# Performance work log

Hardware: AMD Instinct MI355X
Metric: run time of the kernel (lower is better)

The kernel has to match this reference:

```python
import jax, jax.numpy as jnp
import numpy as np

N_NODES = 50000
N_EDGES = 800000
IN_DIM = 128
HID = 32
HEADS = 4
EMB = 64
NEG_SLOPE = 0.2
LN_EPS = 1e-5


def setup_inputs() -> dict:
    key = jax.random.key(0)
    ks = jax.random.split(key, 16)
    s = 0.1
    inp = {
        'x': jax.random.normal(ks[0], (N_NODES, IN_DIM), dtype=jnp.float32),
        'edge_index': jax.random.randint(ks[1], (2, N_EDGES), 0, N_NODES, dtype=jnp.int64),
        # GATConv 1: in=128 -> heads=4, out_per_head=32, concat -> 128
        'W1': jax.random.normal(ks[2], (IN_DIM, HEADS * HID), dtype=jnp.float32) * s,
        'att_src1': jax.random.normal(ks[3], (HEADS, HID), dtype=jnp.float32) * s,
        'att_dst1': jax.random.normal(ks[4], (HEADS, HID), dtype=jnp.float32) * s,
        'b1': jnp.zeros((HEADS * HID,), dtype=jnp.float32),
        'gamma1': jnp.ones((HEADS * HID,), dtype=jnp.float32),
        'beta1': jnp.zeros((HEADS * HID,), dtype=jnp.float32),
        # GATConv 2: in=128 -> heads=1, out=64, concat=False
        'W2': jax.random.normal(ks[5], (HEADS * HID, EMB), dtype=jnp.float32) * s,
        'att_src2': jax.random.normal(ks[6], (1, EMB), dtype=jnp.float32) * s,
        'att_dst2': jax.random.normal(ks[7], (1, EMB), dtype=jnp.float32) * s,
        'b2': jnp.zeros((EMB,), dtype=jnp.float32),
        'gamma2': jnp.ones((EMB,), dtype=jnp.float32),
        'beta2': jnp.zeros((EMB,), dtype=jnp.float32),
    }
    return inp


def _gat_conv(x, src, dst, W, att_src, att_dst):
    # x: [N, F_in]; src/dst: [E'] (self loops included); W: [F_in, H*C]
    N = x.shape[0]
    H, C = att_src.shape
    h = (x @ W).reshape(N, H, C)                          # [N, H, C]
    a_s = jnp.sum(h * att_src, axis=-1)                   # [N, H]
    a_d = jnp.sum(h * att_dst, axis=-1)                   # [N, H]
    e = jax.nn.leaky_relu(a_s[src] + a_d[dst], NEG_SLOPE) # [E', H]
    # segment softmax over destination-node neighborhoods
    m = jax.ops.segment_max(e, dst, num_segments=N)       # [N, H]
    ex = jnp.exp(e - m[dst])
    den = jax.ops.segment_sum(ex, dst, num_segments=N)    # [N, H]
    alpha = ex / den[dst]                                  # [E', H]
    msg = h[src] * alpha[:, :, None]                       # [E', H, C]
    return jax.ops.segment_sum(msg, dst, num_segments=N)  # [N, H, C]


def _layer_norm(x, gamma, beta):
    mu = jnp.mean(x, axis=-1, keepdims=True)
    var = jnp.var(x, axis=-1, keepdims=True)
    return (x - mu) * jax.lax.rsqrt(var + LN_EPS) * gamma + beta


def reference(x, edge_index, W1, att_src1, att_dst1, b1, gamma1, beta1,
              W2, att_src2, att_dst2, b2, gamma2, beta2):
    N = x.shape[0]
    loops = jnp.arange(N, dtype=edge_index.dtype)
    src = jnp.concatenate([edge_index[0], loops])  # PyG add_self_loops=True
    dst = jnp.concatenate([edge_index[1], loops])

    # gat1: heads=4, concat=True
    h1 = _gat_conv(x, src, dst, W1, att_src1, att_dst1)   # [N, 4, 32]
    h1 = h1.reshape(N, -1) + b1                            # [N, 128]
    h1 = jax.nn.relu(_layer_norm(h1, gamma1, beta1))
    # dropout is identity in eval mode

    # gat2: heads=1, concat=False (mean over the single head)
    h2 = _gat_conv(h1, src, dst, W2, att_src2, att_dst2)  # [N, 1, 64]
    h2 = h2.mean(axis=1) + b2                              # [N, 64]
    return _layer_norm(h2, gamma2, beta2)
```

## Files before the change

### kernel.cpp

```cpp
#include <hip/hip_runtime.h>
#include <hip/hip_bf16.h>
#include <math.h>

#define N_NODES 50000
#define N_EDGES 800000
#define HEADS 4
#define HID 32
#define D1 128
#define D2 64
#define NEG_SLOPE 0.2f
#define LN_EPS 1e-5f

#define NB_SCAN ((N_NODES + 255) / 256)
#define CAP 64
#define GB1N 782
#define GB2N 782
#define DEGB 784
#define ILV (2 * GB1N)

typedef __attribute__((ext_vector_type(8))) short bf16x8;
typedef __attribute__((ext_vector_type(4))) float f32x4;

__device__ __forceinline__ float lrelu(float x) { return x > 0.f ? x : NEG_SLOPE * x; }
__device__ __forceinline__ float bf2f(__hip_bfloat16 v) { return __bfloat162float(v); }

__device__ __forceinline__ short f2bf_s(float x) {
    union { __hip_bfloat16 h; short s; } u;
    u.h = __float2bfloat16(x);
    return u.s;
}
__device__ __forceinline__ float bfs2f(short s) {
    union { unsigned u; float f; } v;
    v.u = ((unsigned)(unsigned short)s) << 16;
    return v.f;
}
__device__ __forceinline__ void split_bf(float x, short& hi, short& lo) {
    hi = f2bf_s(x);
    lo = f2bf_s(x - bfs2f(hi));
}

__global__ __launch_bounds__(256) void wprep_kernel(const float* __restrict__ W1,
                                                    const float* __restrict__ W2,
                                                    short* __restrict__ W1h, short* __restrict__ W1l,
                                                    short* __restrict__ W2h, short* __restrict__ W2l) {
    int idx = blockIdx.x * 256 + threadIdx.x;
    if (idx < 16384) {
        int s = idx & 7, l = (idx >> 3) & 63, fid = idx >> 9;
        int kt = fid & 3, nt = fid >> 2;
        int k = kt * 32 + (l >> 4) * 8 + s;
        int n = nt * 16 + (l & 15);
        short hi, lo;
        split_bf(W1[k * 128 + n], hi, lo);
        W1h[idx] = hi;
        W1l[idx] = lo;
    } else if (idx < 16384 + 8192) {
        int j = idx - 16384;
        int s = j & 7, l = (j >> 3) & 63, fid = j >> 9;
        int kt = fid & 3, nt = fid >> 2;
        int k = kt * 32 + (l >> 4) * 8 + s;
        int n = nt * 16 + (l & 15);
        short hi, lo;
        split_bf(W2[k * 64 + n], hi, lo);
        W2h[j] = hi;
        W2l[j] = lo;
    }
}

__global__ __launch_bounds__(256, 3) void gemm1_mfma_degree_kernel(
    const float* __restrict__ X, const short* __restrict__ Wh, const short* __restrict__ Wl,
    __hip_bfloat16* __restrict__ Y,
    const float* __restrict__ att_src, const float* __restrict__ att_dst,
    float* __restrict__ a_s, float* __restrict__ a_d,
    const int* __restrict__ dst, int* __restrict__ deg, int* __restrict__ rank) {
    int bid = blockIdx.x;
    bool isdeg;
    int id;
    if (bid < ILV) {
        isdeg = (bid & 1);
        id = bid >> 1;
    } else {
        isdeg = true;
        id = bid - ILV + GB1N;
    }
    if (isdeg) {
        int t0 = id * 256 + threadIdx.x;
        const int stride = DEGB * 256;
#pragma unroll
        for (int u = 0; u < 4; ++u) {
            int i = t0 + u * stride;
            if (i < N_EDGES) rank[i] = atomicAdd(&deg[dst[i]], 1);
        }
        return;
    }

    int tid = threadIdx.x;
    int w = tid >> 6;
    int l = tid & 63;
    int lr = l & 15;
    int lq = l >> 4;

    const bf16x8* Wh8 = (const bf16x8*)Wh;
    const bf16x8* Wl8 = (const bf16x8*)Wl;
    bf16x8 bh[2][4], bl[2][4];
#pragma unroll
    for (int nt = 0; nt < 2; ++nt)
#pragma unroll
        for (int kt = 0; kt < 4; ++kt) {
            int fid = (2 * w + nt) * 4 + kt;
            bh[nt][kt] = Wh8[fid * 64 + l];
            bl[nt][kt] = Wl8[fid * 64 + l];
        }

    int r0 = id * 64;
    float asv0 = att_src[w * 32 + lr], asv1 = att_src[w * 32 + 16 + lr];
    float adv0 = att_dst[w * 32 + lr], adv1 = att_dst[w * 32 + 16 + lr];

#pragma unroll
    for (int mt = 0; mt < 4; ++mt) {
        int rb = r0 + mt * 16;
        int row = rb + lr;
        if (row >= N_NODES) row = N_NODES - 1;
        const float* xr = X + (size_t)row * 128;
        f32x4 acc0 = {0.f, 0.f, 0.f, 0.f};
        f32x4 acc1 = {0.f, 0.f, 0.f, 0.f};
#pragma unroll
        for (int kt = 0; kt < 4; ++kt) {
            int cb = kt * 32 + lq * 8;
            float4 f0 = *(const float4*)(xr + cb);
            float4 f1 = *(const float4*)(xr + cb + 4);
            float xs[8] = {f0.x, f0.y, f0.z, f0.w, f1.x, f1.y, f1.z, f1.w};
            bf16x8 ah, al;
#pragma unroll
            for (int s = 0; s < 8; ++s) {
                short h_, l_;
                split_bf(xs[s], h_, l_);
                ah[s] = h_;
                al[s] = l_;
            }
            acc0 = __builtin_amdgcn_mfma_f32_16x16x32_bf16(ah, bh[0][kt], acc0, 0, 0, 0);
            acc1 = __builtin_amdgcn_mfma_f32_16x16x32_bf16(ah, bh[1][kt], acc1, 0, 0, 0);
            acc0 = __builtin_amdgcn_mfma_f32_16x16x32_bf16(al, bh[0][kt], acc0, 0, 0, 0);
            acc1 = __builtin_amdgcn_mfma_f32_16x16x32_bf16(al, bh[1][kt], acc1, 0, 0, 0);
            acc0 = __builtin_amdgcn_mfma_f32_16x16x32_bf16(ah, bl[0][kt], acc0, 0, 0, 0);
            acc1 = __builtin_amdgcn_mfma_f32_16x16x32_bf16(ah, bl[1][kt], acc1, 0, 0, 0);
        }
#pragma unroll
        for (int reg = 0; reg < 4; ++reg) {
            int r = rb + lq * 4 + reg;
            float v0 = acc0[reg], v1 = acc1[reg];
            float ps = v0 * asv0 + v1 * asv1;
            float pd = v0 * adv0 + v1 * adv1;
#pragma unroll
            for (int m = 1; m < 16; m <<= 1) {
                ps += __shfl_xor(ps, m, 64);
                pd += __shfl_xor(pd, m, 64);
            }
            if (r < N_NODES) {
                Y[(size_t)r * 128 + w * 32 + lr] = __float2bfloat16(v0);
                Y[(size_t)r * 128 + w * 32 + 16 + lr] = __float2bfloat16(v1);
                if (lr == 0) {
                    a_s[r * 4 + w] = ps;
                    a_d[r * 4 + w] = pd;
                }
            }
        }
    }
}

__global__ __launch_bounds__(256, 3) void gemm2_mfma_kernel(
    const float* __restrict__ X, const short* __restrict__ Wh, const short* __restrict__ Wl,
    __hip_bfloat16* __restrict__ Y,
    const float* __restrict__ att_src, const float* __restrict__ att_dst,
    float* __restrict__ a_s, float* __restrict__ a_d) {
    __shared__ float psh[4][64];
    __shared__ float pdh[4][64];
    int tid = threadIdx.x;
    int w = tid >> 6;
    int l = tid & 63;
    int lr = l & 15;
    int lq = l >> 4;

    const bf16x8* Wh8 = (const bf16x8*)Wh;
    const bf16x8* Wl8 = (const bf16x8*)Wl;
    bf16x8 bh[4], bl[4];
#pragma unroll
    for (int kt = 0; kt < 4; ++kt) {
        int fid = w * 4 + kt;
        bh[kt] = Wh8[fid * 64 + l];
        bl[kt] = Wl8[fid * 64 + l];
    }

    int r0 = blockIdx.x * 64;
    float asv = att_src[w * 16 + lr];
    float adv = att_dst[w * 16 + lr];

    f32x4 acc[4];
#pragma unroll
    for (int mt = 0; mt < 4; ++mt) acc[mt] = (f32x4){0.f, 0.f, 0.f, 0.f};

#pragma unroll
    for (int mt = 0; mt < 4; ++mt) {
        int row = r0 + mt * 16 + lr;
        if (row >= N_NODES) row = N_NODES - 1;
        const float* xr = X + (size_t)row * 128;
#pragma unroll
        for (int kt = 0; kt < 4; ++kt) {
            int cb = kt * 32 + lq * 8;
            float4 f0 = *(const float4*)(xr + cb);
            float4 f1 = *(const float4*)(xr + cb + 4);
            float xs[8] = {f0.x, f0.y, f0.z, f0.w, f1.x, f1.y, f1.z, f1.w};
            bf16x8 ah, al;
#pragma unroll
            for (int s = 0; s < 8; ++s) {
                short h_, l_;
                split_bf(xs[s], h_, l_);
                ah[s] = h_;
                al[s] = l_;
            }
            acc[mt] = __builtin_amdgcn_mfma_f32_16x16x32_bf16(ah, bh[kt], acc[mt], 0, 0, 0);
            acc[mt] = __builtin_amdgcn_mfma_f32_16x16x32_bf16(al, bh[kt], acc[mt], 0, 0, 0);
            acc[mt] = __builtin_amdgcn_mfma_f32_16x16x32_bf16(ah, bl[kt], acc[mt], 0, 0, 0);
        }
    }

#pragma unroll
    for (int mt = 0; mt < 4; ++mt) {
#pragma unroll
        for (int reg = 0; reg < 4; ++reg) {
            int r = r0 + mt * 16 + lq * 4 + reg;
            float v = acc[mt][reg];
            float ps = v * asv;
            float pd = v * adv;
#pragma unroll
            for (int m = 1; m < 16; m <<= 1) {
                ps += __shfl_xor(ps, m, 64);
                pd += __shfl_xor(pd, m, 64);
            }
            if (r < N_NODES) Y[(size_t)r * 64 + w * 16 + lr] = __float2bfloat16(v);
            if (lr == 0) {
                psh[w][mt * 16 + lq * 4 + reg] = ps;
                pdh[w][mt * 16 + lq * 4 + reg] = pd;
            }
        }
    }
    __syncthreads();
    if (tid < 64) {
        int r = r0 + tid;
        if (r < N_NODES) {
            a_s[r] = psh[0][tid] + psh[1][tid] + psh[2][tid] + psh[3][tid];
            a_d[r] = pdh[0][tid] + pdh[1][tid] + pdh[2][tid] + pdh[3][tid];
        }
    }
}

__global__ __launch_bounds__(256) void scan1_kernel(const int* __restrict__ deg,
                                                    int* __restrict__ rpl,
                                                    int* __restrict__ bsum) {
    int i = blockIdx.x * 256 + threadIdx.x;
    int v = (i < N_NODES) ? deg[i] : 0;
    int lane = threadIdx.x & 63;
    int w = threadIdx.x >> 6;
    int x = v;
#pragma unroll
    for (int off = 1; off < 64; off <<= 1) {
        int t = __shfl_up(x, off, 64);
        if (lane >= off) x += t;
    }
    __shared__ int wsum[4];
    if (lane == 63) wsum[w] = x;
    __syncthreads();
    int wo = 0;
    if (w > 0) wo += wsum[0];
    if (w > 1) wo += wsum[1];
    if (w > 2) wo += wsum[2];
    if (i <= N_NODES) rpl[i] = x - v + wo;
    if (threadIdx.x == 255) bsum[blockIdx.x] = x + wo;
}

__global__ __launch_bounds__(256) void scan2_kernel(const int* __restrict__ bsum,
                                                    int* __restrict__ boff) {
    int i = threadIdx.x;
    int v = (i < NB_SCAN) ? bsum[i] : 0;
    int lane = threadIdx.x & 63;
    int w = threadIdx.x >> 6;
    int x = v;
#pragma unroll
    for (int off = 1; off < 64; off <<= 1) {
        int t = __shfl_up(x, off, 64);
        if (lane >= off) x += t;
    }
    __shared__ int wsum[4];
    if (lane == 63) wsum[w] = x;
    __syncthreads();
    int wo = 0;
    if (w > 0) wo += wsum[0];
    if (w > 1) wo += wsum[1];
    if (w > 2) wo += wsum[2];
    if (i < NB_SCAN) boff[i] = x - v + wo;
}

__global__ __launch_bounds__(256) void scatter_kernel(const int* __restrict__ src,
                                                      const int* __restrict__ dst,
                                                      const int* __restrict__ rpl,
                                                      const int* __restrict__ boff,
                                                      const int* __restrict__ rank,
                                                      int* __restrict__ col) {
    int i = blockIdx.x * blockDim.x + threadIdx.x;
    if (i < N_EDGES) {
        int d = dst[i];
        int pos = rpl[d] + boff[d >> 8] + rank[i];
        col[pos] = src[i];
    }
}

__global__ __launch_bounds__(256) void agg1_kernel(const __hip_bfloat16* __restrict__ h,
                                                   const float* __restrict__ a_s,
                                                   const float* __restrict__ a_d,
                                                   const int* __restrict__ rpl,
                                                   const int* __restrict__ boff,
                                                   const int* __restrict__ col,
                                                   const float* __restrict__ b1,
                                                   const float* __restrict__ gamma,
                                                   const float* __restrict__ beta,
                                                   float* __restrict__ out) {
    __shared__ int colsh[4][CAP];
    __shared__ float wsh[4][CAP * 4];
    int wv = threadIdx.x >> 6;
    int lane = threadIdx.x & 63;
    int n = blockIdx.x * 4 + wv;
    int nn = (n < N_NODES) ? n : N_NODES - 1;
    int head = lane >> 4;
    int c = 2 * lane;

    const float4 ad4 = *(const float4*)&a_d[nn * 4];
    int beg = rpl[nn] + boff[nn >> 8];
    int end = rpl[nn + 1] + boff[(nn + 1) >> 8];
    int deg = end - beg;

    float den0 = 0.f, den1 = 0.f, den2 = 0.f, den3 = 0.f;
    for (int t = lane; t < deg; t += 64) {
        int s = col[beg + t];
        const float4 as4 = *(const float4*)&a_s[s * 4];
        float w0 = __expf(lrelu(as4.x + ad4.x));
        float w1 = __expf(lrelu(as4.y + ad4.y));
        float w2 = __expf(lrelu(as4.z + ad4.z));
        float w3 = __expf(lrelu(as4.w + ad4.w));
        if (t < CAP) {
            colsh[wv][t] = s;
            *(float4*)&wsh[wv][t * 4] = make_float4(w0, w1, w2, w3);
        }
        den0 += w0; den1 += w1; den2 += w2; den3 += w3;
    }
#pragma unroll
    for (int m = 1; m < 64; m <<= 1) {
        den0 += __shfl_xor(den0, m, 64);
        den1 += __shfl_xor(den1, m, 64);
        den2 += __shfl_xor(den2, m, 64);
        den3 += __shfl_xor(den3, m, 64);
    }
    float adh = (head == 0) ? ad4.x : (head == 1) ? ad4.y : (head == 2) ? ad4.z : ad4.w;
    float wself = __expf(lrelu(a_s[nn * 4 + head] + adh));
    float den = ((head == 0) ? den0 : (head == 1) ? den1 : (head == 2) ? den2 : den3) + wself;

    __syncthreads();

    float ax0 = 0.f, ay0 = 0.f, ax1 = 0.f, ay1 = 0.f;
    int m0 = (deg < CAP) ? deg : CAP;
    int j = 0;
    for (; j + 3 < m0; j += 4) {
        int s0 = colsh[wv][j + 0], s1 = colsh[wv][j + 1];
        int s2 = colsh[wv][j + 2], s3 = colsh[wv][j + 3];
        float w0 = wsh[wv][(j + 0) * 4 + head], w1 = wsh[wv][(j + 1) * 4 + head];
        float w2 = wsh[wv][(j + 2) * 4 + head], w3 = wsh[wv][(j + 3) * 4 + head];
        __hip_bfloat162 h0 = ((const __hip_bfloat162*)h)[(size_t)s0 * 64 + lane];
        __hip_bfloat162 h1 = ((const __hip_bfloat162*)h)[(size_t)s1 * 64 + lane];
        __hip_bfloat162 h2v = ((const __hip_bfloat162*)h)[(size_t)s2 * 64 + lane];
        __hip_bfloat162 h3 = ((const __hip_bfloat162*)h)[(size_t)s3 * 64 + lane];
        ax0 += w0 * bf2f(h0.x); ay0 += w0 * bf2f(h0.y);
        ax1 += w1 * bf2f(h1.x); ay1 += w1 * bf2f(h1.y);
        ax0 += w2 * bf2f(h2v.x); ay0 += w2 * bf2f(h2v.y);
        ax1 += w3 * bf2f(h3.x); ay1 += w3 * bf2f(h3.y);
    }
    for (; j < m0; ++j) {
        int s = colsh[wv][j];
        float w = wsh[wv][j * 4 + head];
        __hip_bfloat162 hv = ((const __hip_bfloat162*)h)[(size_t)s * 64 + lane];
        ax0 += w * bf2f(hv.x); ay0 += w * bf2f(hv.y);
    }
    for (; j < deg; ++j) {
        int s = col[beg + j];
        float w = __expf(lrelu(a_s[s * 4 + head] + adh));
        __hip_bfloat162 hv = ((const __hip_bfloat162*)h)[(size_t)s * 64 + lane];
        ax0 += w * bf2f(hv.x); ay0 += w * bf2f(hv.y);
    }
    {
        __hip_bfloat162 hv = ((const __hip_bfloat162*)h)[(size_t)nn * 64 + lane];
        ax0 += wself * bf2f(hv.x); ay0 += wself * bf2f(hv.y);
    }
    float inv = 1.f / den;
    float vx = (ax0 + ax1) * inv + b1[c];
    float vy = (ay0 + ay1) * inv + b1[c + 1];

    float s1 = vx + vy, s2 = vx * vx + vy * vy;
#pragma unroll
    for (int m = 1; m < 64; m <<= 1) {
        s1 += __shfl_xor(s1, m, 64);
        s2 += __shfl_xor(s2, m, 64);
    }
    float mean = s1 * (1.f / 128.f);
    float var = s2 * (1.f / 128.f) - mean * mean;
    float r = rsqrtf(var + LN_EPS);
    float ox = fmaxf(0.f, (vx - mean) * r * gamma[c] + beta[c]);
    float oy = fmaxf(0.f, (vy - mean) * r * gamma[c + 1] + beta[c + 1]);
    if (n < N_NODES) *(float2*)&out[(size_t)n * 128 + c] = make_float2(ox, oy);
}

__global__ __launch_bounds__(256) void agg2_kernel(const __hip_bfloat16* __restrict__ h,
                                                   const float* __restrict__ a_s,
                                                   const float* __restrict__ a_d,
                                                   const int* __restrict__ rpl,
                                                   const int* __restrict__ boff,
                                                   const int* __restrict__ col,
                                                   const float* __restrict__ b2,
                                                   const float* __restrict__ gamma,
                                                   const float* __restrict__ beta,
                                                   float* __restrict__ out) {
    __shared__ int colsh[4][CAP];
    __shared__ float wsh[4][CAP];
    int wv = threadIdx.x >> 6;
    int lane = threadIdx.x & 63;
    int n = blockIdx.x * 4 + wv;
    int nn = (n < N_NODES) ? n : N_NODES - 1;

    float adh = a_d[nn];
    int beg = rpl[nn] + boff[nn >> 8];
    int end = rpl[nn + 1] + boff[(nn + 1) >> 8];
    int deg = end - beg;

    float den = 0.f;
    for (int t = lane; t < deg; t += 64) {
        int s = col[beg + t];
        float w = __expf(lrelu(a_s[s] + adh));
        if (t < CAP) {
            colsh[wv][t] = s;
            wsh[wv][t] = w;
        }
        den += w;
    }
#pragma unroll
    for (int m = 1; m < 64; m <<= 1) den += __shfl_xor(den, m, 64);
    float wself = __expf(lrelu(a_s[nn] + adh));
    den += wself;

    __syncthreads();

    float a0 = 0.f, a1 = 0.f;
    int m0 = (deg < CAP) ? deg : CAP;
    int j = 0;
    for (; j + 3 < m0; j += 4) {
        int s0 = colsh[wv][j + 0], s1 = colsh[wv][j + 1];
        int s2 = colsh[wv][j + 2], s3 = colsh[wv][j + 3];
        float w0 = wsh[wv][j + 0], w1 = wsh[wv][j + 1];
        float w2 = wsh[wv][j + 2], w3 = wsh[wv][j + 3];
        a0 += w0 * bf2f(h[(size_t)s0 * 64 + lane]);
        a1 += w1 * bf2f(h[(size_t)s1 * 64 + lane]);
        a0 += w2 * bf2f(h[(size_t)s2 * 64 + lane]);
        a1 += w3 * bf2f(h[(size_t)s3 * 64 + lane]);
    }
    for (; j < m0; ++j) {
        a0 += wsh[wv][j] * bf2f(h[(size_t)colsh[wv][j] * 64 + lane]);
    }
    for (; j < deg; ++j) {
        int s = col[beg + j];
        float w = __expf(lrelu(a_s[s] + adh));
        a0 += w * bf2f(h[(size_t)s * 64 + lane]);
    }
    a0 += wself * bf2f(h[(size_t)nn * 64 + lane]);

    float v = (a0 + a1) / den + b2[lane];

    float s1 = v, s2 = v * v;
#pragma unroll
    for (int m = 1; m < 64; m <<= 1) {
        s1 += __shfl_xor(s1, m, 64);
        s2 += __shfl_xor(s2, m, 64);
    }
    float mean = s1 * (1.f / 64.f);
    float var = s2 * (1.f / 64.f) - mean * mean;
    float r = rsqrtf(var + LN_EPS);
    if (n < N_NODES) out[(size_t)n * 64 + lane] = (v - mean) * r * gamma[lane] + beta[lane];
}

extern "C" void kernel_launch(void* const* d_in, const int* in_sizes, int n_in,
                              void* d_out, int out_size, void* d_ws, size_t ws_size,
                              hipStream_t stream) {
    const float* x        = (const float*)d_in[0];
    const int*   ei       = (const int*)d_in[1];
    const float* W1       = (const float*)d_in[2];
    const float* att_src1 = (const float*)d_in[3];
    const float* att_dst1 = (const float*)d_in[4];
    const float* b1       = (const float*)d_in[5];
    const float* gamma1   = (const float*)d_in[6];
    const float* beta1    = (const float*)d_in[7];
    const float* W2       = (const float*)d_in[8];
    const float* att_src2 = (const float*)d_in[9];
    const float* att_dst2 = (const float*)d_in[10];
    const float* b2       = (const float*)d_in[11];
    const float* gamma2   = (const float*)d_in[12];
    const float* beta2    = (const float*)d_in[13];
    const int* src = ei;
    const int* dst = ei + N_EDGES;
    float* out = (float*)d_out;

    char* ws = (char*)d_ws;
    size_t off = 0;
    auto alloc = [&](size_t bytes) -> void* {
        void* p = ws + off;
        off += bytes;
        off = (off + 255) & ~(size_t)255;
        return p;
    };
    __hip_bfloat16* h1pre = (__hip_bfloat16*)alloc((size_t)N_NODES * 128 * 2);
    __hip_bfloat16* h2pre = (__hip_bfloat16*)alloc((size_t)N_NODES * 64 * 2);
    float* a_s1   = (float*)alloc((size_t)N_NODES * 4 * 4);
    float* a_d1   = (float*)alloc((size_t)N_NODES * 4 * 4);
    float* h1n    = (float*)alloc((size_t)N_NODES * 128 * 4);
    float* a_s2   = (float*)alloc((size_t)N_NODES * 4);
    float* a_d2   = (float*)alloc((size_t)N_NODES * 4);
    int* deg      = (int*)alloc((size_t)N_NODES * 4);
    int* rpl      = (int*)alloc((size_t)(N_NODES + 1) * 4);
    int* col      = (int*)alloc((size_t)N_EDGES * 4);
    int* rank     = (int*)alloc((size_t)N_EDGES * 4);
    int* bsum     = (int*)alloc((size_t)NB_SCAN * 4);
    int* boff     = (int*)alloc((size_t)NB_SCAN * 4);
    short* W1h    = (short*)alloc((size_t)16384 * 2);
    short* W1l    = (short*)alloc((size_t)16384 * 2);
    short* W2h    = (short*)alloc((size_t)8192 * 2);
    short* W2l    = (short*)alloc((size_t)8192 * 2);

    hipMemsetAsync(deg, 0, (size_t)N_NODES * 4, stream);

    const int EB = (N_EDGES + 255) / 256;
    const int NWB = (N_NODES + 3) / 4;

    wprep_kernel<<<96, 256, 0, stream>>>(W1, W2, W1h, W1l, W2h, W2l);

    gemm1_mfma_degree_kernel<<<GB1N + DEGB, 256, 0, stream>>>(
        x, W1h, W1l, h1pre, att_src1, att_dst1, a_s1, a_d1, dst, deg, rank);
    scan1_kernel<<<NB_SCAN, 256, 0, stream>>>(deg, rpl, bsum);
    scan2_kernel<<<1, 256, 0, stream>>>(bsum, boff);
    scatter_kernel<<<EB, 256, 0, stream>>>(src, dst, rpl, boff, rank, col);

    agg1_kernel<<<NWB, 256, 0, stream>>>(h1pre, a_s1, a_d1, rpl, boff, col, b1, gamma1, beta1, h1n);

    gemm2_mfma_kernel<<<GB2N, 256, 0, stream>>>(
        h1n, W2h, W2l, h2pre, att_src2, att_dst2, a_s2, a_d2);
    agg2_kernel<<<NWB, 256, 0, stream>>>(h2pre, a_s2, a_d2, rpl, boff, col, b2, gamma2, beta2, out);
}
```

Measured before the change: 249.6 us.

## Replace global-atomic degree count with per-chunk LDS histograms and sorted scatter

The CSR build drops the per-edge global atomicAdd on degree counts and the per-edge rank array. It now uses 256 edge chunks, each building a packed 16-bit-per-node histogram in shared memory, a column-wise exclusive scan across chunks, and a scatter that re-runs the LDS atomics to get local ranks. The goal is to remove global atomic contention and the rank write/read traffic. In exchange it adds a 25.6 MB histogram buffer that is written, scanned and read again, and the degree computation is no longer interleaved with gemm1.

```diff
diff --git a/kernel.cpp b/kernel.cpp
--- a/kernel.cpp
+++ b/kernel.cpp
@@ -15,8 +15,11 @@
 #define CAP 64
 #define GB1N 782
 #define GB2N 782
-#define DEGB 784
-#define ILV (2 * GB1N)
+
+#define NCHUNK 256
+#define CHE (N_EDGES / NCHUNK)
+#define HWORDS (N_NODES / 2)
+#define HVEC (HWORDS / 4)
 
 typedef __attribute__((ext_vector_type(8))) short bf16x8;
 typedef __attribute__((ext_vector_type(4))) float f32x4;
@@ -66,33 +69,61 @@
     }
 }
 
-__global__ __launch_bounds__(256, 3) void gemm1_mfma_degree_kernel(
+__global__ __launch_bounds__(512) void hist_kernel(const int* __restrict__ dst,
+                                                   unsigned* __restrict__ hist) {
+    __shared__ unsigned cnt[HWORDS];
+    int c = blockIdx.x;
+    for (int i = threadIdx.x; i < HVEC; i += 512) ((uint4*)cnt)[i] = make_uint4(0, 0, 0, 0);
+    __syncthreads();
+    int base = c * CHE;
+    for (int t = threadIdx.x; t < CHE; t += 512) {
+        int d = dst[base + t];
+        atomicAdd(&cnt[d >> 1], 1u << ((d & 1) * 16));
+    }
+    __syncthreads();
+    uint4* out = (uint4*)(hist + (size_t)c * HWORDS);
+    for (int i = threadIdx.x; i < HVEC; i += 512) out[i] = ((const uint4*)cnt)[i];
+}
+
+__global__ __launch_bounds__(256) void chunkscan_kernel(unsigned* __restrict__ hist,
+                                                        unsigned* __restrict__ degp) {
+    int w = blockIdx.x * 256 + threadIdx.x;
+    if (w >= HWORDS) return;
+    unsigned run = 0;
+#pragma unroll 8
+    for (int c = 0; c < NCHUNK; ++c) {
+        unsigned v = hist[(size_t)c * HWORDS + w];
+        hist[(size_t)c * HWORDS + w] = run;
+        run += v;
+    }
+    degp[w] = run;
+}
+
+__global__ __launch_bounds__(512) void scatter_sorted_kernel(const int* __restrict__ src,
+                                                             const int* __restrict__ dst,
+                                                             const unsigned* __restrict__ hist,
+                                                             const int* __restrict__ rpl,
+                                                             const int* __restrict__ boff,
+                                                             int* __restrict__ col) {
+    __shared__ unsigned cnt[HWORDS];
+    int c = blockIdx.x;
+    const uint4* row = (const uint4*)(hist + (size_t)c * HWORDS);
+    for (int i = threadIdx.x; i < HVEC; i += 512) ((uint4*)cnt)[i] = row[i];
+    __syncthreads();
+    int base = c * CHE;
+    for (int t = threadIdx.x; t < CHE; t += 512) {
+        int d = dst[base + t];
+        unsigned old = atomicAdd(&cnt[d >> 1], 1u << ((d & 1) * 16));
+        unsigned r = (old >> ((d & 1) * 16)) & 0xffffu;
+        col[rpl[d] + boff[d >> 8] + (int)r] = src[base + t];
+    }
+}
+
+__global__ __launch_bounds__(256, 3) void gemm1_mfma_kernel(
     const float* __restrict__ X, const short* __restrict__ Wh, const short* __restrict__ Wl,
     __hip_bfloat16* __restrict__ Y,
     const float* __restrict__ att_src, const float* __restrict__ att_dst,
-    float* __restrict__ a_s, float* __restrict__ a_d,
-    const int* __restrict__ dst, int* __restrict__ deg, int* __restrict__ rank) {
-    int bid = blockIdx.x;
-    bool isdeg;
-    int id;
-    if (bid < ILV) {
-        isdeg = (bid & 1);
-        id = bid >> 1;
-    } else {
-        isdeg = true;
-        id = bid - ILV + GB1N;
-    }
-    if (isdeg) {
-        int t0 = id * 256 + threadIdx.x;
-        const int stride = DEGB * 256;
-#pragma unroll
-        for (int u = 0; u < 4; ++u) {
-            int i = t0 + u * stride;
-            if (i < N_EDGES) rank[i] = atomicAdd(&deg[dst[i]], 1);
-        }
-        return;
-    }
-
+    float* __restrict__ a_s, float* __restrict__ a_d) {
     int tid = threadIdx.x;
     int w = tid >> 6;
     int l = tid & 63;
@@ -111,7 +142,7 @@
             bl[nt][kt] = Wl8[fid * 64 + l];
         }
 
-    int r0 = id * 64;
+    int r0 = blockIdx.x * 64;
     float asv0 = att_src[w * 32 + lr], asv1 = att_src[w * 32 + 16 + lr];
     float adv0 = att_dst[w * 32 + lr], adv1 = att_dst[w * 32 + 16 + lr];
 
@@ -253,11 +284,12 @@
     }
 }
 
-__global__ __launch_bounds__(256) void scan1_kernel(const int* __restrict__ deg,
+__global__ __launch_bounds__(256) void scan1_kernel(const unsigned* __restrict__ degp,
                                                     int* __restrict__ rpl,
                                                     int* __restrict__ bsum) {
     int i = blockIdx.x * 256 + threadIdx.x;
-    int v = (i < N_NODES) ? deg[i] : 0;
+    int v = 0;
+    if (i < N_NODES) v = (int)((degp[i >> 1] >> ((i & 1) * 16)) & 0xffffu);
     int lane = threadIdx.x & 63;
     int w = threadIdx.x >> 6;
     int x = v;
@@ -297,20 +329,6 @@
     if (w > 1) wo += wsum[1];
     if (w > 2) wo += wsum[2];
     if (i < NB_SCAN) boff[i] = x - v + wo;
-}
-
-__global__ __launch_bounds__(256) void scatter_kernel(const int* __restrict__ src,
-                                                      const int* __restrict__ dst,
-                                                      const int* __restrict__ rpl,
-                                                      const int* __restrict__ boff,
-                                                      const int* __restrict__ rank,
-                                                      int* __restrict__ col) {
-    int i = blockIdx.x * blockDim.x + threadIdx.x;
-    if (i < N_EDGES) {
-        int d = dst[i];
-        int pos = rpl[d] + boff[d >> 8] + rank[i];
-        col[pos] = src[i];
-    }
 }
 
 __global__ __launch_bounds__(256) void agg1_kernel(const __hip_bfloat16* __restrict__ h,
@@ -527,10 +545,10 @@
     float* h1n    = (float*)alloc((size_t)N_NODES * 128 * 4);
     float* a_s2   = (float*)alloc((size_t)N_NODES * 4);
     float* a_d2   = (float*)alloc((size_t)N_NODES * 4);
-    int* deg      = (int*)alloc((size_t)N_NODES * 4);
+    unsigned* hist = (unsigned*)alloc((size_t)NCHUNK * HWORDS * 4);
+    unsigned* degp = (unsigned*)alloc((size_t)HWORDS * 4);
     int* rpl      = (int*)alloc((size_t)(N_NODES + 1) * 4);
     int* col      = (int*)alloc((size_t)N_EDGES * 4);
-    int* rank     = (int*)alloc((size_t)N_EDGES * 4);
     int* bsum     = (int*)alloc((size_t)NB_SCAN * 4);
     int* boff     = (int*)alloc((size_t)NB_SCAN * 4);
     short* W1h    = (short*)alloc((size_t)16384 * 2);
@@ -538,18 +556,17 @@
     short* W2h    = (short*)alloc((size_t)8192 * 2);
     short* W2l    = (short*)alloc((size_t)8192 * 2);
 
-    hipMemsetAsync(deg, 0, (size_t)N_NODES * 4, stream);
-
-    const int EB = (N_EDGES + 255) / 256;
     const int NWB = (N_NODES + 3) / 4;
 
     wprep_kernel<<<96, 256, 0, stream>>>(W1, W2, W1h, W1l, W2h, W2l);
 
-    gemm1_mfma_degree_kernel<<<GB1N + DEGB, 256, 0, stream>>>(
-        x, W1h, W1l, h1pre, att_src1, att_dst1, a_s1, a_d1, dst, deg, rank);
-    scan1_kernel<<<NB_SCAN, 256, 0, stream>>>(deg, rpl, bsum);
+    hist_kernel<<<NCHUNK, 512, 0, stream>>>(dst, hist);
+    gemm1_mfma_kernel<<<GB1N, 256, 0, stream>>>(
+        x, W1h, W1l, h1pre, att_src1, att_dst1, a_s1, a_d1);
+    chunkscan_kernel<<<(HWORDS + 255) / 256, 256, 0, stream>>>(hist, degp);
+    scan1_kernel<<<NB_SCAN, 256, 0, stream>>>(degp, rpl, bsum);
     scan2_kernel<<<1, 256, 0, stream>>>(bsum, boff);
-    scatter_kernel<<<EB, 256, 0, stream>>>(src, dst, rpl, boff, rank, col);
+    scatter_sorted_kernel<<<NCHUNK, 512, 0, stream>>>(src, dst, hist, rpl, boff, col);
 
     agg1_kernel<<<NWB, 256, 0, stream>>>(h1pre, a_s1, a_d1, rpl, boff, col, b1, gamma1, beta1, h1n);
 
```

Measured after the change: 262.1 us. +5.0%, slower.
